# Performance work log

Measured on AMD Instinct MI355X. Metric: run time of the kernel, lower is better.

The kernel has to match this reference:

```python
import jax, jax.numpy as jnp
import numpy as np

H = 1024  # hidden_dim; GRU hidden size is H+1, embedding_dim = 2*H


def _bigru_scan(h0, Wih_f, Whh_f, bih_f, bhh_f, Wih_b, Whh_b, bih_b, bhh_b):
    """h0: (T, 2, H+1). Runs the per-token recurrence of AnswerSynthesisEncoder.

    At each step the torch code feeds the previous step's output y (2H+2,) back
    in as the GRU *input* x = y[:2H].reshape(2,H).sum(0), and uses the token
    embedding (+f_s,f_e) reshaped to (2, H+1) as the initial hidden state h_0
    of the bidirectional, seq_len=1 GRU. Since h_0 does not depend on the
    carry, the hidden-side gate preactivations are precomputed as one GEMM.
    """
    Hh = H + 1
    gh_f = h0[:, 0] @ Whh_f.T + bhh_f  # (T, 3*(H+1))
    gh_b = h0[:, 1] @ Whh_b.T + bhh_b

    def cell(x, h, gh, Wih, bih):
        gi = Wih @ x + bih
        i_r, i_z, i_n = jnp.split(gi, 3)
        h_r, h_z, h_n = jnp.split(gh, 3)
        r = jax.nn.sigmoid(i_r + h_r)
        z = jax.nn.sigmoid(i_z + h_z)
        n = jnp.tanh(i_n + r * h_n)
        return (1.0 - z) * n + z * h

    def step(y, inp):
        h0_t, ghf_t, ghb_t = inp
        x = y[: 2 * H].reshape(2, H).sum(axis=0)  # (H,)
        yf = cell(x, h0_t[0], ghf_t, Wih_f, bih_f)
        yb = cell(x, h0_t[1], ghb_t, Wih_b, bih_b)
        y_new = jnp.concatenate([yf, yb])  # (2H+2,)
        return y_new, y_new

    y0 = jnp.zeros(2 * Hh, dtype=h0.dtype)
    _, outs = jax.lax.scan(step, y0, (h0, gh_f, gh_b))  # (T, 2H+2)
    # final slice: reshape(2, H+1)[:, :H] per token -> concat of both halves' first H
    return jnp.concatenate([outs[:, :H], outs[:, Hh : Hh + H]], axis=1)  # (T, 2H)


def setup_inputs() -> dict:
    key = jax.random.key(0)
    ks = jax.random.split(key, 12)
    Hh = H + 1
    s = 0.02
    return {
        "e_q": jax.random.normal(ks[0], (512, 2 * H), jnp.float32),
        "e_p": jax.random.normal(ks[1], (4096, 2 * H), jnp.float32),
        "f_s": jax.random.uniform(ks[2], (4096, 1), jnp.float32),
        "f_e": jax.random.uniform(ks[3], (4096, 1), jnp.float32),
        "Wih_f": jax.random.normal(ks[4], (3 * Hh, H), jnp.float32) * s,
        "Whh_f": jax.random.normal(ks[5], (3 * Hh, Hh), jnp.float32) * s,
        "bih_f": jax.random.normal(ks[6], (3 * Hh,), jnp.float32) * s,
        "bhh_f": jax.random.normal(ks[7], (3 * Hh,), jnp.float32) * s,
        "Wih_b": jax.random.normal(ks[8], (3 * Hh, H), jnp.float32) * s,
        "Whh_b": jax.random.normal(ks[9], (3 * Hh, Hh), jnp.float32) * s,
        "bih_b": jax.random.normal(ks[10], (3 * Hh,), jnp.float32) * s,
        "bhh_b": jax.random.normal(ks[11], (3 * Hh,), jnp.float32) * s,
    }


def reference(e_q, e_p, f_s, f_e, Wih_f, Whh_f, bih_f, bhh_f, Wih_b, Whh_b, bih_b, bhh_b):
    Hh = H + 1
    # h_0 per passage token: cat([e_p_t, f_s_t, f_e_t]).reshape(2, H+1)
    h0_p = jnp.concatenate([e_p, f_s, f_e], axis=1).reshape(-1, 2, Hh)
    # h_0 per query token: cat([e_q_t, 0, 0]).reshape(2, H+1)
    zq = jnp.zeros((e_q.shape[0], 2), e_q.dtype)
    h0_q = jnp.concatenate([e_q, zq], axis=1).reshape(-1, 2, Hh)
    h_p = _bigru_scan(h0_p, Wih_f, Whh_f, bih_f, bhh_f, Wih_b, Whh_b, bih_b, bhh_b)
    h_q = _bigru_scan(h0_q, Wih_f, Whh_f, bih_f, bhh_f, Wih_b, Whh_b, bih_b, bhh_b)
    return (h_q, h_p)
```

## Files before the change

kernel.cpp:

```cpp
#include <hip/hip_runtime.h>
#include <stdint.h>


#define H   1024
#define HH  1025
#define N3  3075
#define TQ  512
#define TP  4096
#define MTOT 4608
#define GTOT 2050
#define GH_ELEMS (MTOT * N3)

typedef unsigned long long ull;
typedef __attribute__((ext_vector_type(8))) short short8;
typedef __attribute__((ext_vector_type(4))) float f32x4;

__device__ __forceinline__ float sigm(float x) { return 1.f / (1.f + __expf(-x)); }
__device__ __forceinline__ float fast_tanh(float x) {
    float e = __expf(2.f * x);
    return (e - 1.f) / (e + 1.f);
}

__device__ __forceinline__ unsigned short f2bf(float f) {
    unsigned u = __float_as_uint(f);
    unsigned r = (u + 0x7FFFu + ((u >> 16) & 1u)) >> 16;
    return (unsigned short)r;
}
__device__ __forceinline__ float bf2f(unsigned short h) {
    return __uint_as_float(((unsigned)h) << 16);
}

__global__ __launch_bounds__(256, 2) void gh_gemm_mfma(
    const float* __restrict__ eq, const float* __restrict__ ep,
    const float* __restrict__ fs, const float* __restrict__ fe,
    const float* __restrict__ Whh_f, const float* __restrict__ bhh_f,
    const float* __restrict__ Whh_b, const float* __restrict__ bhh_b,
    float* __restrict__ ghf, float* __restrict__ ghb)
{
    const int dir = blockIdx.z;
    const float* W  = dir ? Whh_b : Whh_f;
    const float* bh = dir ? bhh_b : bhh_f;
    float* gh = dir ? ghb : ghf;
    const int n0 = blockIdx.x * 128;
    const int m0 = blockIdx.y * 64;
    const int tid  = threadIdx.x;
    const int wave = tid >> 6;
    const int lane = tid & 63;

    __shared__ __align__(16) unsigned short Ah[64][40];
    __shared__ __align__(16) unsigned short Al[64][40];
    __shared__ __align__(16) unsigned short Bs[128][40];

    f32x4 acc[8];
#pragma unroll
    for (int c = 0; c < 8; c++) acc[c] = (f32x4){0.f, 0.f, 0.f, 0.f};

    for (int kc = 0; kc < 33; kc++) {
        const int k0 = kc * 32;
#pragma unroll
        for (int u = 0; u < 8; u++) {
            int lin = u * 256 + tid;
            int row = lin >> 5, k = lin & 31;
            int gm = m0 + row, gk = k0 + k;
            float v = 0.f;
            if (gk < HH) {
                bool isq = gm < TQ;
                const float* e = isq ? eq : ep;
                int t = isq ? gm : gm - TQ;
                if (dir == 0)            v = e[(size_t)t * 2048 + gk];
                else if (gk < 1023)      v = e[(size_t)t * 2048 + 1025 + gk];
                else if (!isq)           v = (gk == 1023) ? fs[t] : fe[t];
            }
            unsigned short h = f2bf(v);
            Ah[row][k] = h;
            Al[row][k] = f2bf(v - bf2f(h));
        }
#pragma unroll
        for (int u = 0; u < 16; u++) {
            int lin = u * 256 + tid;
            int r = lin >> 5, k = lin & 31;
            int gr = n0 + r, gk = k0 + k;
            float v = (gr < N3 && gk < HH) ? W[(size_t)gr * HH + gk] : 0.f;
            Bs[r][k] = f2bf(v);
        }
        __syncthreads();

        const int arow = wave * 16 + (lane & 15);
        const int koff = (lane >> 4) * 8;
        short8 ah = *(const short8*)&Ah[arow][koff];
        short8 al = *(const short8*)&Al[arow][koff];
#pragma unroll
        for (int c = 0; c < 8; c++) {
            short8 b = *(const short8*)&Bs[c * 16 + (lane & 15)][koff];
            acc[c] = __builtin_amdgcn_mfma_f32_16x16x32_bf16(ah, b, acc[c], 0, 0, 0);
            acc[c] = __builtin_amdgcn_mfma_f32_16x16x32_bf16(al, b, acc[c], 0, 0, 0);
        }
        __syncthreads();
    }

#pragma unroll
    for (int c = 0; c < 8; c++) {
        int col = n0 + c * 16 + (lane & 15);
        if (col < N3) {
            float bias = bh[col];
#pragma unroll
            for (int r = 0; r < 4; r++) {
                int row = m0 + wave * 16 + (lane >> 4) * 4 + r;
                gh[(size_t)row * N3 + col] = acc[c][r] + bias;
            }
        }
    }
}

__global__ __launch_bounds__(256, 1) void bigru_scan(
    const float* __restrict__ eq, const float* __restrict__ ep,
    const float* __restrict__ fs, const float* __restrict__ fe,
    const float* __restrict__ Wih_f, const float* __restrict__ bih_f,
    const float* __restrict__ Wih_b, const float* __restrict__ bih_b,
    const float* __restrict__ ghf, const float* __restrict__ ghb,
    ull* __restrict__ comm,
    float* __restrict__ out)
{
    __shared__ float xsh[2][2][1024];

    const int tid  = threadIdx.x;
    const int wave = tid >> 6;
    const int lane = tid & 63;
    const int gbase = blockIdx.x * 12 + wave * 3;

    float wreg[9][16];
    float breg[9];
    int   dre[3], je[3];
    bool  vale[3];
#pragma unroll
    for (int e = 0; e < 3; e++) {
        int g = gbase + e;
        bool v = (g < GTOT);
        int gc = v ? g : 0;
        int dir = gc / HH;
        int j = gc % HH;
        dre[e] = dir; je[e] = j; vale[e] = v;
        const float* Wih = dir ? Wih_b : Wih_f;
        const float* bih = dir ? bih_b : bih_f;
#pragma unroll
        for (int gate = 0; gate < 3; gate++) {
            const float* wr = Wih + (size_t)(gate * HH + j) * H;
#pragma unroll
            for (int i = 0; i < 4; i++) {
                float4 w4 = *(const float4*)(wr + i * 256 + lane * 4);
                wreg[e * 3 + gate][i * 4 + 0] = w4.x;
                wreg[e * 3 + gate][i * 4 + 1] = w4.y;
                wreg[e * 3 + gate][i * 4 + 2] = w4.z;
                wreg[e * 3 + gate][i * 4 + 3] = w4.w;
            }
            breg[e * 3 + gate] = bih[gate * HH + j];
        }
    }

    int sgh[3], sh0[3], sspec[3];
#pragma unroll
    for (int e = 0; e < 3; e++) {
        sgh[e]   = __builtin_amdgcn_readfirstlane(dre[e] * GH_ELEMS + je[e]);
        sh0[e]   = __builtin_amdgcn_readfirstlane(dre[e] ? (1025 + je[e]) : je[e]);
        sspec[e] = __builtin_amdgcn_readfirstlane(
                       (dre[e] && je[e] >= 1023) ? (je[e] - 1022) : 0);
    }
    const float* ghAll = ghf;

    float ghcP[9], h0cP[3], ghcQ[9], h0cQ[3];

    auto loadP = [&](int tt, float gh9[9], float h03[3]) {
        size_t base = (size_t)(TQ + tt) * N3;
#pragma unroll
        for (int e = 0; e < 3; e++) {
#pragma unroll
            for (int gate = 0; gate < 3; gate++)
                gh9[e * 3 + gate] = ghAll[base + (size_t)sgh[e] + gate * HH];
            h03[e] = (sspec[e] == 0) ? ep[(size_t)tt * 2048 + sh0[e]]
                   : (sspec[e] == 1) ? fs[tt] : fe[tt];
        }
    };
    auto loadQ = [&](int tt, float gh9[9], float h03[3]) {
        size_t base = (size_t)tt * N3;
#pragma unroll
        for (int e = 0; e < 3; e++) {
#pragma unroll
            for (int gate = 0; gate < 3; gate++)
                gh9[e * 3 + gate] = ghAll[base + (size_t)sgh[e] + gate * HH];
            h03[e] = (sspec[e] == 0) ? eq[(size_t)tt * 2048 + sh0[e]] : 0.f;
        }
    };

    loadP(0, ghcP, h0cP);
    loadQ(0, ghcQ, h0cQ);

    ull* commP = comm;
    ull* commQ = comm + 2 * GTOT;

    for (int t = 0; t < TP; t++) {
        const bool doq = (t < TQ);
        const int par = t & 1;

        if (t == 0) {
#pragma unroll
            for (int u = 0; u < 4; u++) {
                int j = tid + 256 * u;
                xsh[par][0][j] = 0.f;
                xsh[par][1][j] = 0.f;
            }
        } else {
            const int slot = (t + 1) & 1;
            const unsigned tag = (unsigned)t;
            ull* cp = commP + slot * GTOT;
            ull* cq = commQ + slot * GTOT;
            int idx[8];
#pragma unroll
            for (int u = 0; u < 4; u++) {
                int j = tid + 256 * u;
                idx[2 * u]     = j;
                idx[2 * u + 1] = (j == 0) ? 1024 : (1025 + j - 1);
            }
            ull vp[8], vq[8];
#pragma unroll
            for (int u = 0; u < 8; u++)
                vp[u] = __hip_atomic_load(&cp[idx[u]], __ATOMIC_RELAXED, __HIP_MEMORY_SCOPE_AGENT);
            if (doq) {
#pragma unroll
                for (int u = 0; u < 8; u++)
                    vq[u] = __hip_atomic_load(&cq[idx[u]], __ATOMIC_RELAXED, __HIP_MEMORY_SCOPE_AGENT);
            }
            bool done = false;
            while (!done) {
                done = true;
#pragma unroll
                for (int u = 0; u < 8; u++) {
                    if ((unsigned)(vp[u] >> 32) != tag) {
                        done = false;
                        vp[u] = __hip_atomic_load(&cp[idx[u]], __ATOMIC_RELAXED, __HIP_MEMORY_SCOPE_AGENT);
                    }
                }
                if (doq) {
#pragma unroll
                    for (int u = 0; u < 8; u++) {
                        if ((unsigned)(vq[u] >> 32) != tag) {
                            done = false;
                            vq[u] = __hip_atomic_load(&cq[idx[u]], __ATOMIC_RELAXED, __HIP_MEMORY_SCOPE_AGENT);
                        }
                    }
                }
            }
#pragma unroll
            for (int u = 0; u < 4; u++) {
                int j = tid + 256 * u;
                xsh[par][0][j] = __uint_as_float((unsigned)vp[2 * u]) +
                                 __uint_as_float((unsigned)vp[2 * u + 1]);
            }
            if (doq) {
#pragma unroll
                for (int u = 0; u < 4; u++) {
                    int j = tid + 256 * u;
                    xsh[par][1][j] = __uint_as_float((unsigned)vq[2 * u]) +
                                     __uint_as_float((unsigned)vq[2 * u + 1]);
                }
            }
        }
        __syncthreads();

        float ghnP[9], h0nP[3], ghnQ[9], h0nQ[3];
        const bool ldn = (t + 1) < TP;
        const bool ldq = (t + 1) < TQ;
        if (ldn) loadP(t + 1, ghnP, h0nP);
        if (ldq) loadQ(t + 1, ghnQ, h0nQ);

        float accp[9];
        {
            float x[16];
#pragma unroll
            for (int i = 0; i < 4; i++) {
                float4 x4 = *(const float4*)&xsh[par][0][i * 256 + lane * 4];
                x[i * 4 + 0] = x4.x; x[i * 4 + 1] = x4.y;
                x[i * 4 + 2] = x4.z; x[i * 4 + 3] = x4.w;
            }
#pragma unroll
            for (int r = 0; r < 9; r++) {
                float s = 0.f;
#pragma unroll
                for (int i = 0; i < 16; i++) s += wreg[r][i] * x[i];
                accp[r] = s;
            }
        }
#pragma unroll
        for (int r = 0; r < 9; r++) {
            float v = accp[r];
#pragma unroll
            for (int off = 32; off > 0; off >>= 1) v += __shfl_xor(v, off, 64);
            accp[r] = v + breg[r];
        }

        float accq[9];
        if (doq) {
            float x[16];
#pragma unroll
            for (int i = 0; i < 4; i++) {
                float4 x4 = *(const float4*)&xsh[par][1][i * 256 + lane * 4];
                x[i * 4 + 0] = x4.x; x[i * 4 + 1] = x4.y;
                x[i * 4 + 2] = x4.z; x[i * 4 + 3] = x4.w;
            }
#pragma unroll
            for (int r = 0; r < 9; r++) {
                float s = 0.f;
#pragma unroll
                for (int i = 0; i < 16; i++) s += wreg[r][i] * x[i];
#pragma unroll
                for (int off = 32; off > 0; off >>= 1) s += __shfl_xor(s, off, 64);
                accq[r] = s + breg[r];
            }
        }

        const ull tagout = ((ull)(unsigned)(t + 1)) << 32;
        float yP[3], yQ[3];
#pragma unroll
        for (int e = 0; e < 3; e++) {
            float r = sigm(accp[e * 3 + 0] + ghcP[e * 3 + 0]);
            float z = sigm(accp[e * 3 + 1] + ghcP[e * 3 + 1]);
            float n = fast_tanh(accp[e * 3 + 2] + r * ghcP[e * 3 + 2]);
            yP[e] = (1.f - z) * n + z * h0cP[e];
            if (lane == 0 && vale[e]) {
                ull pk = tagout | (ull)__float_as_uint(yP[e]);
                __hip_atomic_store(&commP[par * GTOT + (gbase + e)], pk,
                                   __ATOMIC_RELAXED, __HIP_MEMORY_SCOPE_AGENT);
            }
        }
        if (doq) {
#pragma unroll
            for (int e = 0; e < 3; e++) {
                float r = sigm(accq[e * 3 + 0] + ghcQ[e * 3 + 0]);
                float z = sigm(accq[e * 3 + 1] + ghcQ[e * 3 + 1]);
                float n = fast_tanh(accq[e * 3 + 2] + r * ghcQ[e * 3 + 2]);
                yQ[e] = (1.f - z) * n + z * h0cQ[e];
                if (lane == 0 && vale[e]) {
                    ull pk = tagout | (ull)__float_as_uint(yQ[e]);
                    __hip_atomic_store(&commQ[par * GTOT + (gbase + e)], pk,
                                       __ATOMIC_RELAXED, __HIP_MEMORY_SCOPE_AGENT);
                }
            }
        }
        if (lane == 0) {
#pragma unroll
            for (int e = 0; e < 3; e++) {
                if (vale[e] && je[e] < H) {
                    out[(size_t)TQ * 2048 + (size_t)t * 2048 + dre[e] * H + je[e]] = yP[e];
                    if (doq)
                        out[(size_t)t * 2048 + dre[e] * H + je[e]] = yQ[e];
                }
            }
        }

        if (ldn) {
#pragma unroll
            for (int i = 0; i < 9; i++) ghcP[i] = ghnP[i];
#pragma unroll
            for (int e = 0; e < 3; e++) h0cP[e] = h0nP[e];
        }
        if (ldq) {
#pragma unroll
            for (int i = 0; i < 9; i++) ghcQ[i] = ghnQ[i];
#pragma unroll
            for (int e = 0; e < 3; e++) h0cQ[e] = h0nQ[e];
        }
    }
}

extern "C" void kernel_launch(void* const* d_in, const int* in_sizes, int n_in,
                              void* d_out, int out_size, void* d_ws, size_t ws_size,
                              hipStream_t stream) {
    const float* eq    = (const float*)d_in[0];
    const float* ep    = (const float*)d_in[1];
    const float* fs    = (const float*)d_in[2];
    const float* fe    = (const float*)d_in[3];
    const float* Wih_f = (const float*)d_in[4];
    const float* Whh_f = (const float*)d_in[5];
    const float* bih_f = (const float*)d_in[6];
    const float* bhh_f = (const float*)d_in[7];
    const float* Wih_b = (const float*)d_in[8];
    const float* Whh_b = (const float*)d_in[9];
    const float* bih_b = (const float*)d_in[10];
    const float* bhh_b = (const float*)d_in[11];
    float* out = (float*)d_out;

    const size_t ghElems = (size_t)GH_ELEMS;
    float* ghf = (float*)d_ws;
    float* ghb = ghf + ghElems;
    size_t commOff = ((2 * ghElems * sizeof(float)) + 4095) & ~(size_t)4095;
    ull* comm = (ull*)((char*)d_ws + commOff);

    hipMemsetAsync(comm, 0, (size_t)4 * GTOT * sizeof(ull), stream);

    dim3 ggrid((N3 + 127) / 128, MTOT / 64, 2);
    gh_gemm_mfma<<<ggrid, 256, 0, stream>>>(eq, ep, fs, fe, Whh_f, bhh_f, Whh_b, bhh_b, ghf, ghb);

    bigru_scan<<<dim3(171), dim3(256), 0, stream>>>(
        eq, ep, fs, fe, Wih_f, bih_f, Wih_b, bih_b, ghf, ghb, comm, out);
}
```

Baseline: 14.20 ms.

## Split P/Q waits in scan and add pre-split bf16 GEMM path

The scan loop now waits only on the passage chain's communication slots before computing the P step. It issues the query chain's loads early and spins on them only after the P outputs are published, so the two independent recurrences stop blocking each other. Separately, a prep kernel pre-splits the h0 activations into bf16 hi/lo halves. A new 128x128-tile MFMA GEMM then consumes them, and it runs only when the workspace is large enough. This adds an extra __syncthreads per step during the Q phase and a small extra launch.

Measured after the change: 16.49 ms. 1.16x slower.

```diff
diff --git a/kernel.cpp b/kernel.cpp
--- a/kernel.cpp
+++ b/kernel.cpp
@@ -2,14 +2,16 @@
 #include <stdint.h>
 
 
-#define H   1024
-#define HH  1025
-#define N3  3075
-#define TQ  512
-#define TP  4096
+#define H    1024
+#define HH   1025
+#define N3   3075
+#define TQ   512
+#define TP   4096
 #define MTOT 4608
 #define GTOT 2050
 #define GH_ELEMS (MTOT * N3)
+#define AKP  1056
+#define ATOT ((size_t)MTOT * 2 * AKP)
 
 typedef unsigned long long ull;
 typedef __attribute__((ext_vector_type(8))) short short8;
@@ -20,7 +22,6 @@
     float e = __expf(2.f * x);
     return (e - 1.f) / (e + 1.f);
 }
-
 __device__ __forceinline__ unsigned short f2bf(float f) {
     unsigned u = __float_as_uint(f);
     unsigned r = (u + 0x7FFFu + ((u >> 16) & 1u)) >> 16;
@@ -28,6 +29,125 @@
 }
 __device__ __forceinline__ float bf2f(unsigned short h) {
     return __uint_as_float(((unsigned)h) << 16);
+}
+
+#define ALOAD(p)     __hip_atomic_load((p), __ATOMIC_RELAXED, __HIP_MEMORY_SCOPE_AGENT)
+#define ASTORE(p, v) __hip_atomic_store((p), (v), __ATOMIC_RELAXED, __HIP_MEMORY_SCOPE_AGENT)
+
+__global__ __launch_bounds__(256) void prep_abf(
+    const float* __restrict__ eq, const float* __restrict__ ep,
+    const float* __restrict__ fs, const float* __restrict__ fe,
+    unsigned short* __restrict__ abf)
+{
+    const int K8 = AKP / 8;
+    int idx = blockIdx.x * 256 + threadIdx.x;
+    int rowid = idx / K8;
+    if (rowid >= MTOT * 2) return;
+    int k0 = (idx - rowid * K8) * 8;
+    int dir = rowid & 1;
+    int m = rowid >> 1;
+    bool isq = m < TQ;
+    const float* e = isq ? eq : ep;
+    int t = isq ? m : m - TQ;
+
+    short8 hi, lo;
+#pragma unroll
+    for (int j = 0; j < 8; j++) {
+        int gk = k0 + j;
+        float v = 0.f;
+        if (gk < HH) {
+            if (dir == 0)            v = e[(size_t)t * 2048 + gk];
+            else if (gk < 1023)      v = e[(size_t)t * 2048 + 1025 + gk];
+            else if (!isq)           v = (gk == 1023) ? fs[t] : fe[t];
+        }
+        unsigned short h = f2bf(v);
+        hi[j] = (short)h;
+        lo[j] = (short)f2bf(v - bf2f(h));
+    }
+    size_t base = (size_t)rowid * AKP + k0;
+    *(short8*)&abf[base] = hi;
+    *(short8*)&abf[ATOT + base] = lo;
+}
+
+__global__ __launch_bounds__(256, 2) void gh_gemm_fast(
+    const unsigned short* __restrict__ abf,
+    const float* __restrict__ Whh_f, const float* __restrict__ bhh_f,
+    const float* __restrict__ Whh_b, const float* __restrict__ bhh_b,
+    float* __restrict__ ghf, float* __restrict__ ghb)
+{
+    const int dir = blockIdx.z;
+    const float* W  = dir ? Whh_b : Whh_f;
+    const float* bh = dir ? bhh_b : bhh_f;
+    float* gh = dir ? ghb : ghf;
+    const int n0 = blockIdx.x * 128;
+    const int m0 = blockIdx.y * 128;
+    const int tid = threadIdx.x, wave = tid >> 6, lane = tid & 63;
+
+    __shared__ __align__(16) unsigned short Ah[128][40];
+    __shared__ __align__(16) unsigned short Al[128][40];
+    __shared__ __align__(16) unsigned short Bs[128][40];
+
+    f32x4 acc[2][8];
+#pragma unroll
+    for (int rt = 0; rt < 2; rt++)
+#pragma unroll
+        for (int c = 0; c < 8; c++) acc[rt][c] = (f32x4){0.f, 0.f, 0.f, 0.f};
+
+    for (int kc = 0; kc < 33; kc++) {
+        const int k0 = kc * 32;
+        {
+            int r = tid >> 1, h16 = (tid & 1) * 16;
+            size_t arow = ((size_t)(m0 + r) * 2 + dir) * AKP + k0 + h16;
+            short8 v0 = *(const short8*)&abf[arow];
+            short8 v1 = *(const short8*)&abf[arow + 8];
+            *(short8*)&Ah[r][h16]     = v0;
+            *(short8*)&Ah[r][h16 + 8] = v1;
+            short8 u0 = *(const short8*)&abf[ATOT + arow];
+            short8 u1 = *(const short8*)&abf[ATOT + arow + 8];
+            *(short8*)&Al[r][h16]     = u0;
+            *(short8*)&Al[r][h16 + 8] = u1;
+        }
+#pragma unroll
+        for (int u = 0; u < 16; u++) {
+            int lin = u * 256 + tid;
+            int r = lin >> 5, k = lin & 31;
+            int gr = n0 + r, gk = k0 + k;
+            float v = (gr < N3 && gk < HH) ? W[(size_t)gr * HH + gk] : 0.f;
+            Bs[r][k] = f2bf(v);
+        }
+        __syncthreads();
+
+        const int rA0 = wave * 32 + (lane & 15);
+        const int ko  = (lane >> 4) * 8;
+        short8 ah0 = *(const short8*)&Ah[rA0][ko];
+        short8 ah1 = *(const short8*)&Ah[rA0 + 16][ko];
+        short8 al0 = *(const short8*)&Al[rA0][ko];
+        short8 al1 = *(const short8*)&Al[rA0 + 16][ko];
+#pragma unroll
+        for (int c = 0; c < 8; c++) {
+            short8 b = *(const short8*)&Bs[c * 16 + (lane & 15)][ko];
+            acc[0][c] = __builtin_amdgcn_mfma_f32_16x16x32_bf16(ah0, b, acc[0][c], 0, 0, 0);
+            acc[0][c] = __builtin_amdgcn_mfma_f32_16x16x32_bf16(al0, b, acc[0][c], 0, 0, 0);
+            acc[1][c] = __builtin_amdgcn_mfma_f32_16x16x32_bf16(ah1, b, acc[1][c], 0, 0, 0);
+            acc[1][c] = __builtin_amdgcn_mfma_f32_16x16x32_bf16(al1, b, acc[1][c], 0, 0, 0);
+        }
+        __syncthreads();
+    }
+
+#pragma unroll
+    for (int rt = 0; rt < 2; rt++)
+#pragma unroll
+    for (int c = 0; c < 8; c++) {
+        int col = n0 + c * 16 + (lane & 15);
+        if (col < N3) {
+            float bias = bh[col];
+#pragma unroll
+            for (int j = 0; j < 4; j++) {
+                int row = m0 + wave * 32 + rt * 16 + (lane >> 4) * 4 + j;
+                gh[(size_t)row * N3 + col] = acc[rt][c][j] + bias;
+            }
+        }
+    }
 }
 
 __global__ __launch_bounds__(256, 2) void gh_gemm_mfma(
@@ -197,9 +317,21 @@
     ull* commP = comm;
     ull* commQ = comm + 2 * GTOT;
 
+    int idx[8];
+#pragma unroll
+    for (int u = 0; u < 4; u++) {
+        int j = tid + 256 * u;
+        idx[2 * u]     = j;
+        idx[2 * u + 1] = (j == 0) ? 1024 : (1024 + j);
+    }
+
     for (int t = 0; t < TP; t++) {
         const bool doq = (t < TQ);
         const int par = t & 1;
+        const int slot = (t + 1) & 1;
+        const unsigned tag = (unsigned)t;
+        ull* cp = commP + slot * GTOT;
+        ull* cq = commQ + slot * GTOT;
 
         if (t == 0) {
 #pragma unroll
@@ -209,26 +341,9 @@
                 xsh[par][1][j] = 0.f;
             }
         } else {
-            const int slot = (t + 1) & 1;
-            const unsigned tag = (unsigned)t;
-            ull* cp = commP + slot * GTOT;
-            ull* cq = commQ + slot * GTOT;
-            int idx[8];
-#pragma unroll
-            for (int u = 0; u < 4; u++) {
-                int j = tid + 256 * u;
-                idx[2 * u]     = j;
-                idx[2 * u + 1] = (j == 0) ? 1024 : (1025 + j - 1);
-            }
-            ull vp[8], vq[8];
-#pragma unroll
-            for (int u = 0; u < 8; u++)
-                vp[u] = __hip_atomic_load(&cp[idx[u]], __ATOMIC_RELAXED, __HIP_MEMORY_SCOPE_AGENT);
-            if (doq) {
-#pragma unroll
-                for (int u = 0; u < 8; u++)
-                    vq[u] = __hip_atomic_load(&cq[idx[u]], __ATOMIC_RELAXED, __HIP_MEMORY_SCOPE_AGENT);
-            }
+            ull vp[8];
+#pragma unroll
+            for (int u = 0; u < 8; u++) vp[u] = ALOAD(&cp[idx[u]]);
             bool done = false;
             while (!done) {
                 done = true;
@@ -236,16 +351,7 @@
                 for (int u = 0; u < 8; u++) {
                     if ((unsigned)(vp[u] >> 32) != tag) {
                         done = false;
-                        vp[u] = __hip_atomic_load(&cp[idx[u]], __ATOMIC_RELAXED, __HIP_MEMORY_SCOPE_AGENT);
-                    }
-                }
-                if (doq) {
-#pragma unroll
-                    for (int u = 0; u < 8; u++) {
-                        if ((unsigned)(vq[u] >> 32) != tag) {
-                            done = false;
-                            vq[u] = __hip_atomic_load(&cq[idx[u]], __ATOMIC_RELAXED, __HIP_MEMORY_SCOPE_AGENT);
-                        }
+                        vp[u] = ALOAD(&cp[idx[u]]);
                     }
                 }
             }
@@ -255,16 +361,15 @@
                 xsh[par][0][j] = __uint_as_float((unsigned)vp[2 * u]) +
                                  __uint_as_float((unsigned)vp[2 * u + 1]);
             }
-            if (doq) {
-#pragma unroll
-                for (int u = 0; u < 4; u++) {
-                    int j = tid + 256 * u;
-                    xsh[par][1][j] = __uint_as_float((unsigned)vq[2 * u]) +
-                                     __uint_as_float((unsigned)vq[2 * u + 1]);
-                }
-            }
         }
         __syncthreads();
+
+        ull vq[8];
+        if (doq && t > 0) {
+#pragma unroll
+            for (int u = 0; u < 8; u++) vq[u] = ALOAD(&cq[idx[u]]);
+            __builtin_amdgcn_sched_barrier(0);
+        }
 
         float ghnP[9], h0nP[3], ghnQ[9], h0nQ[3];
         const bool ldn = (t + 1) < TP;
@@ -295,26 +400,6 @@
 #pragma unroll
             for (int off = 32; off > 0; off >>= 1) v += __shfl_xor(v, off, 64);
             accp[r] = v + breg[r];
-        }
-
-        float accq[9];
-        if (doq) {
-            float x[16];
-#pragma unroll
-            for (int i = 0; i < 4; i++) {
-                float4 x4 = *(const float4*)&xsh[par][1][i * 256 + lane * 4];
-                x[i * 4 + 0] = x4.x; x[i * 4 + 1] = x4.y;
-                x[i * 4 + 2] = x4.z; x[i * 4 + 3] = x4.w;
-            }
-#pragma unroll
-            for (int r = 0; r < 9; r++) {
-                float s = 0.f;
-#pragma unroll
-                for (int i = 0; i < 16; i++) s += wreg[r][i] * x[i];
-#pragma unroll
-                for (int off = 32; off > 0; off >>= 1) s += __shfl_xor(s, off, 64);
-                accq[r] = s + breg[r];
-            }
         }
 
         const ull tagout = ((ull)(unsigned)(t + 1)) << 32;
@@ -327,11 +412,51 @@
             yP[e] = (1.f - z) * n + z * h0cP[e];
             if (lane == 0 && vale[e]) {
                 ull pk = tagout | (ull)__float_as_uint(yP[e]);
-                __hip_atomic_store(&commP[par * GTOT + (gbase + e)], pk,
-                                   __ATOMIC_RELAXED, __HIP_MEMORY_SCOPE_AGENT);
-            }
-        }
+                ASTORE(&commP[par * GTOT + (gbase + e)], pk);
+            }
+        }
+
         if (doq) {
+            if (t > 0) {
+                bool done = false;
+                while (!done) {
+                    done = true;
+#pragma unroll
+                    for (int u = 0; u < 8; u++) {
+                        if ((unsigned)(vq[u] >> 32) != tag) {
+                            done = false;
+                            vq[u] = ALOAD(&cq[idx[u]]);
+                        }
+                    }
+                }
+#pragma unroll
+                for (int u = 0; u < 4; u++) {
+                    int j = tid + 256 * u;
+                    xsh[par][1][j] = __uint_as_float((unsigned)vq[2 * u]) +
+                                     __uint_as_float((unsigned)vq[2 * u + 1]);
+                }
+            }
+            __syncthreads();
+
+            float accq[9];
+            {
+                float x[16];
+#pragma unroll
+                for (int i = 0; i < 4; i++) {
+                    float4 x4 = *(const float4*)&xsh[par][1][i * 256 + lane * 4];
+                    x[i * 4 + 0] = x4.x; x[i * 4 + 1] = x4.y;
+                    x[i * 4 + 2] = x4.z; x[i * 4 + 3] = x4.w;
+                }
+#pragma unroll
+                for (int r = 0; r < 9; r++) {
+                    float s = 0.f;
+#pragma unroll
+                    for (int i = 0; i < 16; i++) s += wreg[r][i] * x[i];
+#pragma unroll
+                    for (int off = 32; off > 0; off >>= 1) s += __shfl_xor(s, off, 64);
+                    accq[r] = s + breg[r];
+                }
+            }
 #pragma unroll
             for (int e = 0; e < 3; e++) {
                 float r = sigm(accq[e * 3 + 0] + ghcQ[e * 3 + 0]);
@@ -340,11 +465,11 @@
                 yQ[e] = (1.f - z) * n + z * h0cQ[e];
                 if (lane == 0 && vale[e]) {
                     ull pk = tagout | (ull)__float_as_uint(yQ[e]);
-                    __hip_atomic_store(&commQ[par * GTOT + (gbase + e)], pk,
-                                       __ATOMIC_RELAXED, __HIP_MEMORY_SCOPE_AGENT);
-                }
-            }
-        }
+                    ASTORE(&commQ[par * GTOT + (gbase + e)], pk);
+                }
+            }
+        }
+
         if (lane == 0) {
 #pragma unroll
             for (int e = 0; e < 3; e++) {
@@ -388,16 +513,26 @@
     const float* bhh_b = (const float*)d_in[11];
     float* out = (float*)d_out;
 
-    const size_t ghElems = (size_t)GH_ELEMS;
     float* ghf = (float*)d_ws;
-    float* ghb = ghf + ghElems;
-    size_t commOff = ((2 * ghElems * sizeof(float)) + 4095) & ~(size_t)4095;
+    float* ghb = ghf + (size_t)GH_ELEMS;
+    size_t commOff = ((2 * (size_t)GH_ELEMS * sizeof(float)) + 4095) & ~(size_t)4095;
     ull* comm = (ull*)((char*)d_ws + commOff);
+    size_t abfOff = (commOff + (size_t)4 * GTOT * sizeof(ull) + 4095) & ~(size_t)4095;
+    size_t abfBytes = 2 * ATOT * sizeof(unsigned short);
+    unsigned short* abf = (unsigned short*)((char*)d_ws + abfOff);
+    const bool fastOK = (ws_size >= abfOff + abfBytes);
 
     hipMemsetAsync(comm, 0, (size_t)4 * GTOT * sizeof(ull), stream);
 
-    dim3 ggrid((N3 + 127) / 128, MTOT / 64, 2);
-    gh_gemm_mfma<<<ggrid, 256, 0, stream>>>(eq, ep, fs, fe, Whh_f, bhh_f, Whh_b, bhh_b, ghf, ghb);
+    if (fastOK) {
+        int prepBlocks = (MTOT * 2 * (AKP / 8) + 255) / 256;
+        prep_abf<<<dim3(prepBlocks), 256, 0, stream>>>(eq, ep, fs, fe, abf);
+        gh_gemm_fast<<<dim3((N3 + 127) / 128, MTOT / 128, 2), 256, 0, stream>>>(
+            abf, Whh_f, bhh_f, Whh_b, bhh_b, ghf, ghb);
+    } else {
+        gh_gemm_mfma<<<dim3((N3 + 127) / 128, MTOT / 64, 2), 256, 0, stream>>>(
+            eq, ep, fs, fe, Whh_f, bhh_f, Whh_b, bhh_b, ghf, ghb);
+    }
 
     bigru_scan<<<dim3(171), dim3(256), 0, stream>>>(
         eq, ep, fs, fe, Wih_f, bih_f, Wih_b, bih_b, ghf, ghb, comm, out);
```
